# Kernel tuning notes

Measured on AMD Instinct MI355X. Metric: run time of the kernel, lower is better.

The kernel has to match this reference:

```python
import jax, jax.numpy as jnp
import numpy as np

B, N, D, H, DH = 2, 2048, 1024, 16, 64  # batch, seq, dim, heads, dim_head


def setup_inputs() -> dict:
    key = jax.random.key(0)
    ks = jax.random.split(key, 5)
    x = jax.random.normal(ks[0], (B, N, D), dtype=jnp.float32)
    Wq = jax.random.normal(ks[1], (D, H * DH), dtype=jnp.float32) * 0.02
    Wk = jax.random.normal(ks[2], (D, H * DH), dtype=jnp.float32) * 0.02
    Wv = jax.random.normal(ks[3], (D, H * DH), dtype=jnp.float32) * 0.02
    Wo = jax.random.normal(ks[4], (H * DH, D), dtype=jnp.float32) * 0.02
    bo = jnp.zeros((D,), dtype=jnp.float32)
    return {"x": x, "Wq": Wq, "Wk": Wk, "Wv": Wv, "Wo": Wo, "bo": bo}


def reference(x, Wq, Wk, Wv, Wo, bo):
    b, n, _ = x.shape
    scale = DH ** -0.5
    q = (x @ Wq).reshape(b, n, H, DH)
    k = (x @ Wk).reshape(b, n, H, DH)
    v = (x @ Wv).reshape(b, n, H, DH)
    # ALiBi slopes: 1 / (256**(1/H))**(h+1), per get_alibi_slope
    base = (2.0 ** 8) ** (1.0 / H)
    slope = 1.0 / base ** jnp.arange(1, H + 1, dtype=jnp.float32)  # [H]
    pos = jnp.arange(n, dtype=jnp.float32)
    # q_bias=[slope, slope*i], k_bias=[-j, 1] -> dot = slope*(i-j)
    bias = slope[:, None, None] * (pos[:, None] - pos[None, :])  # [H, N, N]
    scores = jnp.einsum('bihd,bjhd->bhij', q, k) * scale + bias[None]
    causal = pos[:, None] >= pos[None, :]  # i >= j
    scores = jnp.where(causal[None, None], scores, jnp.float32(-1e30))
    attn = jax.nn.softmax(scores, axis=-1)
    out = jnp.einsum('bhij,bjhd->bihd', attn, v).reshape(b, n, H * DH)
    return out @ Wo + bo
```

## Files before the change

### kernel.cpp

```cpp
#include <hip/hip_runtime.h>
#include <hip/hip_bf16.h>


typedef __bf16 bf16x8 __attribute__((ext_vector_type(8)));
typedef float f32x4 __attribute__((ext_vector_type(4)));
typedef short s4 __attribute__((ext_vector_type(4)));
typedef unsigned short ushort_t;

#define MFMA_16x16x32(a, b, c) __builtin_amdgcn_mfma_f32_16x16x32_bf16(a, b, c, 0, 0, 0)
#define MFMA16(a, b, c) __builtin_amdgcn_mfma_f32_16x16x16bf16_1k(a, b, c, 0, 0, 0)

__device__ __forceinline__ ushort_t f2bf(float f) {
    __hip_bfloat16 h = __float2bfloat16(f);
    return __builtin_bit_cast(ushort_t, h);
}
__device__ __forceinline__ float bf2f(ushort_t u) {
    unsigned x = ((unsigned)u) << 16;
    return __builtin_bit_cast(float, x);
}

__device__ __forceinline__ unsigned detect_fp32(const void* wp) {
    const ushort_t* w = (const ushort_t*)wp;
    unsigned c = 0;
    #pragma unroll
    for (int i = 0; i < 128; ++i) c += (((w[i] >> 7) & 0xFF) >= 0x7F) ? 1u : 0u;
    return (c > 8) ? 1u : 0u;
}

__device__ __forceinline__ uint4 load8(const void* p, size_t idx, unsigned flag) {
    if (flag) {
        const float* f = (const float*)p + idx;
        float4 a = *(const float4*)f;
        float4 b = *(const float4*)(f + 4);
        ushort_t u[8] = { f2bf(a.x), f2bf(a.y), f2bf(a.z), f2bf(a.w),
                          f2bf(b.x), f2bf(b.y), f2bf(b.z), f2bf(b.w) };
        return *(uint4*)u;
    }
    return *(const uint4*)((const ushort_t*)p + idx);
}

__global__ __launch_bounds__(256) void convert_x(
    const void* __restrict__ X, const void* __restrict__ Wq, const void* __restrict__ bo,
    ushort_t* __restrict__ Xc, ushort_t* __restrict__ boc)
{
    const unsigned flag = detect_fp32(Wq);
    const int blk = blockIdx.x;
    if (blk < 2048) {
        size_t idx = (size_t)blk * 2048 + (size_t)threadIdx.x * 8;
        *(uint4*)(Xc + idx) = load8(X, idx, flag);
    } else {
        size_t idx = (size_t)threadIdx.x * 8;
        if (idx < 1024) *(uint4*)(boc + idx) = load8(bo, idx, flag);
    }
}

__global__ __launch_bounds__(256) void transpose_w(
    const void* __restrict__ Wq, const void* __restrict__ Wk,
    const void* __restrict__ Wv, const void* __restrict__ Wo,
    ushort_t* __restrict__ WqT, ushort_t* __restrict__ WkT,
    ushort_t* __restrict__ WvT, ushort_t* __restrict__ WoT)
{
    __shared__ ushort_t T[64][72];
    const unsigned flag = detect_fp32(Wq);
    const int z = blockIdx.z;
    const void* W = (z == 0) ? Wq : ((z == 1) ? Wk : ((z == 2) ? Wv : Wo));
    ushort_t* WT = (z == 0) ? WqT : ((z == 1) ? WkT : ((z == 2) ? WvT : WoT));

    const int k0 = blockIdx.y * 64, n0 = blockIdx.x * 64;
    const int r = threadIdx.x >> 2, c = (threadIdx.x & 3) * 16;

    *(uint4*)&T[r][c]     = load8(W, (size_t)(k0 + r) * 1024 + n0 + c,     flag);
    *(uint4*)&T[r][c + 8] = load8(W, (size_t)(k0 + r) * 1024 + n0 + c + 8, flag);
    __syncthreads();
    ushort_t tmp[16];
    #pragma unroll
    for (int j = 0; j < 16; ++j) tmp[j] = T[c + j][r];
    *(uint4*)(WT + (size_t)(n0 + r) * 1024 + k0 + c)     = *(uint4*)&tmp[0];
    *(uint4*)(WT + (size_t)(n0 + r) * 1024 + k0 + c + 8) = *(uint4*)&tmp[8];
}

__global__ __launch_bounds__(256) void qkv_gemm(
    const ushort_t* __restrict__ X, const ushort_t* __restrict__ WqT,
    const ushort_t* __restrict__ WkT, const ushort_t* __restrict__ WvT,
    ushort_t* __restrict__ Q, ushort_t* __restrict__ K, ushort_t* __restrict__ Vt)
{
    __shared__ ushort_t As[128 * 40];
    __shared__ ushort_t Bs[128 * 40];

    const int z = blockIdx.z;
    const ushort_t* WT = (z == 0) ? WqT : ((z == 1) ? WkT : WvT);

    const int tid  = threadIdx.x;
    const int m0   = blockIdx.y * 128, n0 = blockIdx.x * 128;
    const int lane = tid & 63, wv = tid >> 6;
    const int quad = lane >> 4, l15 = lane & 15;
    const int wm = (wv & 1) * 64, wn = (wv >> 1) * 64;
    const int ar = tid >> 1, ac = (tid & 1) * 16;

    f32x4 acc[4][4] = {};

    uint4 ra0 = *(const uint4*)(X  + (size_t)(m0 + ar) * 1024 + ac);
    uint4 ra1 = *(const uint4*)(X  + (size_t)(m0 + ar) * 1024 + ac + 8);
    uint4 rb0 = *(const uint4*)(WT + (size_t)(n0 + ar) * 1024 + ac);
    uint4 rb1 = *(const uint4*)(WT + (size_t)(n0 + ar) * 1024 + ac + 8);

    for (int kt = 0; kt < 32; ++kt) {
        __syncthreads();
        *(uint4*)(As + ar * 40 + ac)     = ra0;
        *(uint4*)(As + ar * 40 + ac + 8) = ra1;
        *(uint4*)(Bs + ar * 40 + ac)     = rb0;
        *(uint4*)(Bs + ar * 40 + ac + 8) = rb1;
        __syncthreads();
        if (kt < 31) {
            int k0 = (kt + 1) * 32;
            ra0 = *(const uint4*)(X  + (size_t)(m0 + ar) * 1024 + k0 + ac);
            ra1 = *(const uint4*)(X  + (size_t)(m0 + ar) * 1024 + k0 + ac + 8);
            rb0 = *(const uint4*)(WT + (size_t)(n0 + ar) * 1024 + k0 + ac);
            rb1 = *(const uint4*)(WT + (size_t)(n0 + ar) * 1024 + k0 + ac + 8);
        }
        bf16x8 af[4], bfr[4];
        #pragma unroll
        for (int t = 0; t < 4; ++t) {
            af[t]  = *(const bf16x8*)(As + (wm + t * 16 + l15) * 40 + quad * 8);
            bfr[t] = *(const bf16x8*)(Bs + (wn + t * 16 + l15) * 40 + quad * 8);
        }
        #pragma unroll
        for (int mt = 0; mt < 4; ++mt)
            #pragma unroll
            for (int nt = 0; nt < 4; ++nt)
                acc[mt][nt] = MFMA_16x16x32(af[mt], bfr[nt], acc[mt][nt]);
    }

    #pragma unroll
    for (int mt = 0; mt < 4; ++mt) {
        #pragma unroll
        for (int nt = 0; nt < 4; ++nt) {
            if (z == 2) {
                int c  = n0 + wn + nt * 16 + l15;
                int h  = c >> 6, dh = c & 63;
                int mA = m0 + wm + mt * 16 + quad * 4;
                int b  = mA >> 11, nseq = mA & 2047;
                ushort_t pk[4];
                #pragma unroll
                for (int r = 0; r < 4; ++r) pk[r] = f2bf(acc[mt][nt][r]);
                *(ushort2*)(Vt + ((size_t)((b * 16 + h) * 64 + dh)) * 2048 + nseq)     = *(ushort2*)&pk[0];
                *(ushort2*)(Vt + ((size_t)((b * 16 + h) * 64 + dh)) * 2048 + nseq + 2) = *(ushort2*)&pk[2];
            } else {
                ushort_t* dst = (z == 0) ? Q : K;
                #pragma unroll
                for (int r = 0; r < 4; ++r) {
                    int m = m0 + wm + mt * 16 + quad * 4 + r;
                    int c = n0 + wn + nt * 16 + l15;
                    int b = m >> 11, nseq = m & 2047;
                    int h = c >> 6, dh = c & 63;
                    dst[((size_t)((b * 16 + h) * 2048 + nseq)) * 64 + dh] = f2bf(acc[mt][nt][r]);
                }
            }
        }
    }
}

__global__ __launch_bounds__(256) void attn_kernel(
    const ushort_t* __restrict__ Q, const ushort_t* __restrict__ K,
    const ushort_t* __restrict__ Vt, ushort_t* __restrict__ AO)
{
    __shared__ ushort_t Ks[64 * 72];
    __shared__ ushort_t Vs[64 * 72];

    const int tid  = threadIdx.x;
    const int wv   = tid >> 6, lane = tid & 63;
    const int quad = lane >> 4, l15 = lane & 15;
    const int bh   = blockIdx.x, h = bh & 15, b = bh >> 4;
    const int qb   = 31 - (int)blockIdx.y;
    const int iw   = qb * 64 + wv * 16;
    const int i_   = iw + l15;

    const ushort_t* Qh = Q  + (size_t)bh * 2048 * 64;
    const ushort_t* Kh = K  + (size_t)bh * 2048 * 64;
    const ushort_t* Vh = Vt + (size_t)bh * 64 * 2048;

    const float LOG2E = 1.44269504088896340736f;
    const float sl2 = exp2f(-0.5f * (float)(h + 1)) * LOG2E;
    const float c1  = 0.125f * LOG2E;

    bf16x8 qf0 = *(const bf16x8*)(Qh + (size_t)(iw + l15) * 64 + quad * 8);
    bf16x8 qf1 = *(const bf16x8*)(Qh + (size_t)(iw + l15) * 64 + 32 + quad * 8);

    s4 onesf;
    #pragma unroll
    for (int e = 0; e < 4; ++e) onesf[e] = (short)0x3F80;

    f32x4 accv[4] = {};
    f32x4 accl = {};

    const int sr = tid >> 2, sc = (tid & 3) * 16;
    const int ntiles = qb + 1;

    uint4 ka0, ka1, va0, va1;
    {
        ka0 = *(const uint4*)(Kh + (size_t)sr * 64 + sc);
        ka1 = *(const uint4*)(Kh + (size_t)sr * 64 + sc + 8);
        va0 = *(const uint4*)(Vh + (size_t)sr * 2048 + sc);
        va1 = *(const uint4*)(Vh + (size_t)sr * 2048 + sc + 8);
    }

    for (int jt = 0; jt < ntiles; ++jt) {
        __syncthreads();
        *(uint4*)(Ks + sr * 72 + sc)     = ka0;
        *(uint4*)(Ks + sr * 72 + sc + 8) = ka1;
        *(uint4*)(Vs + sr * 72 + sc)     = va0;
        *(uint4*)(Vs + sr * 72 + sc + 8) = va1;
        __syncthreads();
        if (jt + 1 < ntiles) {
            int j0n = (jt + 1) * 64;
            ka0 = *(const uint4*)(Kh + (size_t)(j0n + sr) * 64 + sc);
            ka1 = *(const uint4*)(Kh + (size_t)(j0n + sr) * 64 + sc + 8);
            va0 = *(const uint4*)(Vh + (size_t)sr * 2048 + j0n + sc);
            va1 = *(const uint4*)(Vh + (size_t)sr * 2048 + j0n + sc + 8);
        }
        const bool dtile = (jt == qb);
        #pragma unroll
        for (int js = 0; js < 4; ++js) {
            const int j0s = jt * 64 + js * 16;
            if (dtile && j0s > iw + 15) break;
            f32x4 sT = {};
            bf16x8 kf0 = *(const bf16x8*)(Ks + (js * 16 + l15) * 72 + quad * 8);
            bf16x8 kf1 = *(const bf16x8*)(Ks + (js * 16 + l15) * 72 + 32 + quad * 8);
            sT = MFMA_16x16x32(kf0, qf0, sT);
            sT = MFMA_16x16x32(kf1, qf1, sT);
            unsigned u[4];
            #pragma unroll
            for (int r = 0; r < 4; ++r) {
                int j = j0s + quad * 4 + r;
                float p = exp2f(fmaf(sT[r], c1, -sl2 * (float)j));
                if (dtile && j > i_) p = 0.0f;
                u[r] = __builtin_bit_cast(unsigned, p) + 0x8000u;
            }
            uint2 dd = { (u[0] >> 16) | (u[1] & 0xFFFF0000u),
                         (u[2] >> 16) | (u[3] & 0xFFFF0000u) };
            s4 pf = __builtin_bit_cast(s4, dd);
            accl = MFMA16(onesf, pf, accl);
            #pragma unroll
            for (int dt = 0; dt < 4; ++dt) {
                s4 vf = *(const s4*)(Vs + (dt * 16 + l15) * 72 + js * 16 + quad * 4);
                accv[dt] = MFMA16(vf, pf, accv[dt]);
            }
        }
    }

    const float inv = 1.0f / fmaxf(accl[0], 1e-30f);
    const size_t obase = ((size_t)(b * 2048 + i_)) * 1024 + h * 64;
    #pragma unroll
    for (int dt = 0; dt < 4; ++dt) {
        ushort_t pk[4];
        #pragma unroll
        for (int r = 0; r < 4; ++r) pk[r] = f2bf(accv[dt][r] * inv);
        *(ushort2*)(AO + obase + dt * 16 + quad * 4)     = *(ushort2*)&pk[0];
        *(ushort2*)(AO + obase + dt * 16 + quad * 4 + 2) = *(ushort2*)&pk[2];
    }
}

__global__ __launch_bounds__(256) void oproj_gemm(
    const ushort_t* __restrict__ A, const ushort_t* __restrict__ WT,
    const ushort_t* __restrict__ bias, float* __restrict__ out)
{
    __shared__ ushort_t As[128 * 40];
    __shared__ ushort_t Bs[128 * 40];

    const int tid  = threadIdx.x;
    const int m0   = blockIdx.y * 128, n0 = blockIdx.x * 128;
    const int lane = tid & 63, wv = tid >> 6;
    const int quad = lane >> 4, l15 = lane & 15;
    const int wm = (wv & 1) * 64, wn = (wv >> 1) * 64;
    const int ar = tid >> 1, ac = (tid & 1) * 16;

    f32x4 acc[4][4] = {};

    uint4 ra0 = *(const uint4*)(A  + (size_t)(m0 + ar) * 1024 + ac);
    uint4 ra1 = *(const uint4*)(A  + (size_t)(m0 + ar) * 1024 + ac + 8);
    uint4 rb0 = *(const uint4*)(WT + (size_t)(n0 + ar) * 1024 + ac);
    uint4 rb1 = *(const uint4*)(WT + (size_t)(n0 + ar) * 1024 + ac + 8);

    for (int kt = 0; kt < 32; ++kt) {
        __syncthreads();
        *(uint4*)(As + ar * 40 + ac)     = ra0;
        *(uint4*)(As + ar * 40 + ac + 8) = ra1;
        *(uint4*)(Bs + ar * 40 + ac)     = rb0;
        *(uint4*)(Bs + ar * 40 + ac + 8) = rb1;
        __syncthreads();
        if (kt < 31) {
            int k0 = (kt + 1) * 32;
            ra0 = *(const uint4*)(A  + (size_t)(m0 + ar) * 1024 + k0 + ac);
            ra1 = *(const uint4*)(A  + (size_t)(m0 + ar) * 1024 + k0 + ac + 8);
            rb0 = *(const uint4*)(WT + (size_t)(n0 + ar) * 1024 + k0 + ac);
            rb1 = *(const uint4*)(WT + (size_t)(n0 + ar) * 1024 + k0 + ac + 8);
        }
        bf16x8 af[4], bfr[4];
        #pragma unroll
        for (int t = 0; t < 4; ++t) {
            af[t]  = *(const bf16x8*)(As + (wm + t * 16 + l15) * 40 + quad * 8);
            bfr[t] = *(const bf16x8*)(Bs + (wn + t * 16 + l15) * 40 + quad * 8);
        }
        #pragma unroll
        for (int mt = 0; mt < 4; ++mt)
            #pragma unroll
            for (int nt = 0; nt < 4; ++nt)
                acc[mt][nt] = MFMA_16x16x32(af[mt], bfr[nt], acc[mt][nt]);
    }

    #pragma unroll
    for (int mt = 0; mt < 4; ++mt) {
        #pragma unroll
        for (int nt = 0; nt < 4; ++nt) {
            #pragma unroll
            for (int r = 0; r < 4; ++r) {
                int m = m0 + wm + mt * 16 + quad * 4 + r;
                int c = n0 + wn + nt * 16 + l15;
                out[(size_t)m * 1024 + c] = acc[mt][nt][r] + bf2f(bias[c]);
            }
        }
    }
}

extern "C" void kernel_launch(void* const* d_in, const int* in_sizes, int n_in,
                              void* d_out, int out_size, void* d_ws, size_t ws_size,
                              hipStream_t stream) {
    const void* X  = d_in[0];
    const void* Wq = d_in[1];
    const void* Wk = d_in[2];
    const void* Wv = d_in[3];
    const void* Wo = d_in[4];
    const void* bo = d_in[5];

    const size_t M = 1024 * 1024;
    ushort_t* ws  = (ushort_t*)d_ws;
    ushort_t* Qb  = ws;
    ushort_t* Kb  = ws + 4 * M;
    ushort_t* Vt  = ws + 8 * M;
    ushort_t* Xc  = ws + 12 * M;
    ushort_t* AO  = ws + 12 * M;
    ushort_t* WqT = ws + 16 * M;
    ushort_t* WkT = ws + 17 * M;
    ushort_t* WvT = ws + 18 * M;
    ushort_t* WoT = ws + 19 * M;
    ushort_t* boc = ws + 20 * M;
    float* out = (float*)d_out;

    convert_x<<<2049, 256, 0, stream>>>(X, Wq, bo, Xc, boc);
    transpose_w<<<dim3(16, 16, 4), 256, 0, stream>>>(Wq, Wk, Wv, Wo, WqT, WkT, WvT, WoT);
    qkv_gemm<<<dim3(8, 32, 3), 256, 0, stream>>>(Xc, WqT, WkT, WvT, Qb, Kb, Vt);
    attn_kernel<<<dim3(32, 32), 256, 0, stream>>>(Qb, Kb, Vt, AO);
    oproj_gemm<<<dim3(8, 32), 256, 0, stream>>>(AO, WoT, boc, out);
}
```

Baseline: 198.0 us.

## Load GEMM tiles directly into LDS with XOR swizzle and split causal diagonal path

Both projection GEMMs now stage tiles with global_load_lds, copying straight from global memory into an unpadded, XOR-swizzled LDS layout instead of passing through registers. This frees registers and avoids the padded layout. It also gives up the register prefetch of the next tile, so each iteration waits on its own loads with no overlap. The attention kernel splits off the diagonal tile so each wave runs only its needed subtiles, with masking applied only on the last one.

```diff
diff --git a/kernel.cpp b/kernel.cpp
--- a/kernel.cpp
+++ b/kernel.cpp
@@ -17,6 +17,12 @@
 __device__ __forceinline__ float bf2f(ushort_t u) {
     unsigned x = ((unsigned)u) << 16;
     return __builtin_bit_cast(float, x);
+}
+
+__device__ __forceinline__ void gl_lds16(const ushort_t* g, ushort_t* l) {
+    __builtin_amdgcn_global_load_lds(
+        (const __attribute__((address_space(1))) void*)g,
+        (__attribute__((address_space(3))) void*)l, 16, 0, 0);
 }
 
 __device__ __forceinline__ unsigned detect_fp32(const void* wp) {
@@ -84,8 +90,8 @@
     const ushort_t* __restrict__ WkT, const ushort_t* __restrict__ WvT,
     ushort_t* __restrict__ Q, ushort_t* __restrict__ K, ushort_t* __restrict__ Vt)
 {
-    __shared__ ushort_t As[128 * 40];
-    __shared__ ushort_t Bs[128 * 40];
+    __shared__ ushort_t As[128 * 32];
+    __shared__ ushort_t Bs[128 * 32];
 
     const int z = blockIdx.z;
     const ushort_t* WT = (z == 0) ? WqT : ((z == 1) ? WkT : WvT);
@@ -95,34 +101,32 @@
     const int lane = tid & 63, wv = tid >> 6;
     const int quad = lane >> 4, l15 = lane & 15;
     const int wm = (wv & 1) * 64, wn = (wv >> 1) * 64;
-    const int ar = tid >> 1, ac = (tid & 1) * 16;
+
+    const int lrow = lane >> 2;
+    const int schk = (lane & 3) ^ ((lane >> 3) & 3);
+    const int ra0_ = wv * 16 + lrow;
+    ushort_t* aB0 = As + wv * 512;
+    ushort_t* aB1 = As + 2048 + wv * 512;
+    ushort_t* bB0 = Bs + wv * 512;
+    ushort_t* bB1 = Bs + 2048 + wv * 512;
+    const int sp = quad ^ ((l15 >> 1) & 3);
 
     f32x4 acc[4][4] = {};
 
-    uint4 ra0 = *(const uint4*)(X  + (size_t)(m0 + ar) * 1024 + ac);
-    uint4 ra1 = *(const uint4*)(X  + (size_t)(m0 + ar) * 1024 + ac + 8);
-    uint4 rb0 = *(const uint4*)(WT + (size_t)(n0 + ar) * 1024 + ac);
-    uint4 rb1 = *(const uint4*)(WT + (size_t)(n0 + ar) * 1024 + ac + 8);
-
     for (int kt = 0; kt < 32; ++kt) {
-        __syncthreads();
-        *(uint4*)(As + ar * 40 + ac)     = ra0;
-        *(uint4*)(As + ar * 40 + ac + 8) = ra1;
-        *(uint4*)(Bs + ar * 40 + ac)     = rb0;
-        *(uint4*)(Bs + ar * 40 + ac + 8) = rb1;
-        __syncthreads();
-        if (kt < 31) {
-            int k0 = (kt + 1) * 32;
-            ra0 = *(const uint4*)(X  + (size_t)(m0 + ar) * 1024 + k0 + ac);
-            ra1 = *(const uint4*)(X  + (size_t)(m0 + ar) * 1024 + k0 + ac + 8);
-            rb0 = *(const uint4*)(WT + (size_t)(n0 + ar) * 1024 + k0 + ac);
-            rb1 = *(const uint4*)(WT + (size_t)(n0 + ar) * 1024 + k0 + ac + 8);
-        }
+        const int k0 = kt * 32;
+        __syncthreads();
+        gl_lds16(X  + (size_t)(m0 + ra0_)      * 1024 + k0 + schk * 8, aB0);
+        gl_lds16(X  + (size_t)(m0 + 64 + ra0_) * 1024 + k0 + schk * 8, aB1);
+        gl_lds16(WT + (size_t)(n0 + ra0_)      * 1024 + k0 + schk * 8, bB0);
+        gl_lds16(WT + (size_t)(n0 + 64 + ra0_) * 1024 + k0 + schk * 8, bB1);
+        __syncthreads();
+
         bf16x8 af[4], bfr[4];
         #pragma unroll
         for (int t = 0; t < 4; ++t) {
-            af[t]  = *(const bf16x8*)(As + (wm + t * 16 + l15) * 40 + quad * 8);
-            bfr[t] = *(const bf16x8*)(Bs + (wn + t * 16 + l15) * 40 + quad * 8);
+            af[t]  = *(const bf16x8*)(As + (wm + t * 16 + l15) * 32 + sp * 8);
+            bfr[t] = *(const bf16x8*)(Bs + (wn + t * 16 + l15) * 32 + sp * 8);
         }
         #pragma unroll
         for (int mt = 0; mt < 4; ++mt)
@@ -196,13 +200,36 @@
     const int sr = tid >> 2, sc = (tid & 3) * 16;
     const int ntiles = qb + 1;
 
-    uint4 ka0, ka1, va0, va1;
-    {
-        ka0 = *(const uint4*)(Kh + (size_t)sr * 64 + sc);
-        ka1 = *(const uint4*)(Kh + (size_t)sr * 64 + sc + 8);
-        va0 = *(const uint4*)(Vh + (size_t)sr * 2048 + sc);
-        va1 = *(const uint4*)(Vh + (size_t)sr * 2048 + sc + 8);
-    }
+    uint4 ka0 = *(const uint4*)(Kh + (size_t)sr * 64 + sc);
+    uint4 ka1 = *(const uint4*)(Kh + (size_t)sr * 64 + sc + 8);
+    uint4 va0 = *(const uint4*)(Vh + (size_t)sr * 2048 + sc);
+    uint4 va1 = *(const uint4*)(Vh + (size_t)sr * 2048 + sc + 8);
+
+    auto subtile = [&](int jt, int js, bool masked) {
+        const int j0s = jt * 64 + js * 16;
+        f32x4 sT = {};
+        bf16x8 kf0 = *(const bf16x8*)(Ks + (js * 16 + l15) * 72 + quad * 8);
+        bf16x8 kf1 = *(const bf16x8*)(Ks + (js * 16 + l15) * 72 + 32 + quad * 8);
+        sT = MFMA_16x16x32(kf0, qf0, sT);
+        sT = MFMA_16x16x32(kf1, qf1, sT);
+        unsigned u[4];
+        #pragma unroll
+        for (int r = 0; r < 4; ++r) {
+            int j = j0s + quad * 4 + r;
+            float p = exp2f(fmaf(sT[r], c1, -sl2 * (float)j));
+            if (masked && j > i_) p = 0.0f;
+            u[r] = __builtin_bit_cast(unsigned, p) + 0x8000u;
+        }
+        uint2 dd = { (u[0] >> 16) | (u[1] & 0xFFFF0000u),
+                     (u[2] >> 16) | (u[3] & 0xFFFF0000u) };
+        s4 pf = __builtin_bit_cast(s4, dd);
+        accl = MFMA16(onesf, pf, accl);
+        #pragma unroll
+        for (int dt = 0; dt < 4; ++dt) {
+            s4 vf = *(const s4*)(Vs + (dt * 16 + l15) * 72 + js * 16 + quad * 4);
+            accv[dt] = MFMA16(vf, pf, accv[dt]);
+        }
+    };
 
     for (int jt = 0; jt < ntiles; ++jt) {
         __syncthreads();
@@ -218,33 +245,12 @@
             va0 = *(const uint4*)(Vh + (size_t)sr * 2048 + j0n + sc);
             va1 = *(const uint4*)(Vh + (size_t)sr * 2048 + j0n + sc + 8);
         }
-        const bool dtile = (jt == qb);
-        #pragma unroll
-        for (int js = 0; js < 4; ++js) {
-            const int j0s = jt * 64 + js * 16;
-            if (dtile && j0s > iw + 15) break;
-            f32x4 sT = {};
-            bf16x8 kf0 = *(const bf16x8*)(Ks + (js * 16 + l15) * 72 + quad * 8);
-            bf16x8 kf1 = *(const bf16x8*)(Ks + (js * 16 + l15) * 72 + 32 + quad * 8);
-            sT = MFMA_16x16x32(kf0, qf0, sT);
-            sT = MFMA_16x16x32(kf1, qf1, sT);
-            unsigned u[4];
+        if (jt < qb) {
             #pragma unroll
-            for (int r = 0; r < 4; ++r) {
-                int j = j0s + quad * 4 + r;
-                float p = exp2f(fmaf(sT[r], c1, -sl2 * (float)j));
-                if (dtile && j > i_) p = 0.0f;
-                u[r] = __builtin_bit_cast(unsigned, p) + 0x8000u;
-            }
-            uint2 dd = { (u[0] >> 16) | (u[1] & 0xFFFF0000u),
-                         (u[2] >> 16) | (u[3] & 0xFFFF0000u) };
-            s4 pf = __builtin_bit_cast(s4, dd);
-            accl = MFMA16(onesf, pf, accl);
-            #pragma unroll
-            for (int dt = 0; dt < 4; ++dt) {
-                s4 vf = *(const s4*)(Vs + (dt * 16 + l15) * 72 + js * 16 + quad * 4);
-                accv[dt] = MFMA16(vf, pf, accv[dt]);
-            }
+            for (int js = 0; js < 4; ++js) subtile(jt, js, false);
+        } else {
+            for (int js = 0; js < wv; ++js) subtile(jt, js, false);
+            subtile(jt, wv, true);
         }
     }
 
@@ -264,42 +270,40 @@
     const ushort_t* __restrict__ A, const ushort_t* __restrict__ WT,
     const ushort_t* __restrict__ bias, float* __restrict__ out)
 {
-    __shared__ ushort_t As[128 * 40];
-    __shared__ ushort_t Bs[128 * 40];
+    __shared__ ushort_t As[128 * 32];
+    __shared__ ushort_t Bs[128 * 32];
 
     const int tid  = threadIdx.x;
     const int m0   = blockIdx.y * 128, n0 = blockIdx.x * 128;
     const int lane = tid & 63, wv = tid >> 6;
     const int quad = lane >> 4, l15 = lane & 15;
     const int wm = (wv & 1) * 64, wn = (wv >> 1) * 64;
-    const int ar = tid >> 1, ac = (tid & 1) * 16;
+
+    const int lrow = lane >> 2;
+    const int schk = (lane & 3) ^ ((lane >> 3) & 3);
+    const int ra0_ = wv * 16 + lrow;
+    ushort_t* aB0 = As + wv * 512;
+    ushort_t* aB1 = As + 2048 + wv * 512;
+    ushort_t* bB0 = Bs + wv * 512;
+    ushort_t* bB1 = Bs + 2048 + wv * 512;
+    const int sp = quad ^ ((l15 >> 1) & 3);
 
     f32x4 acc[4][4] = {};
 
-    uint4 ra0 = *(const uint4*)(A  + (size_t)(m0 + ar) * 1024 + ac);
-    uint4 ra1 = *(const uint4*)(A  + (size_t)(m0 + ar) * 1024 + ac + 8);
-    uint4 rb0 = *(const uint4*)(WT + (size_t)(n0 + ar) * 1024 + ac);
-    uint4 rb1 = *(const uint4*)(WT + (size_t)(n0 + ar) * 1024 + ac + 8);
-
     for (int kt = 0; kt < 32; ++kt) {
-        __syncthreads();
-        *(uint4*)(As + ar * 40 + ac)     = ra0;
-        *(uint4*)(As + ar * 40 + ac + 8) = ra1;
-        *(uint4*)(Bs + ar * 40 + ac)     = rb0;
-        *(uint4*)(Bs + ar * 40 + ac + 8) = rb1;
-        __syncthreads();
-        if (kt < 31) {
-            int k0 = (kt + 1) * 32;
-            ra0 = *(const uint4*)(A  + (size_t)(m0 + ar) * 1024 + k0 + ac);
-            ra1 = *(const uint4*)(A  + (size_t)(m0 + ar) * 1024 + k0 + ac + 8);
-            rb0 = *(const uint4*)(WT + (size_t)(n0 + ar) * 1024 + k0 + ac);
-            rb1 = *(const uint4*)(WT + (size_t)(n0 + ar) * 1024 + k0 + ac + 8);
-        }
+        const int k0 = kt * 32;
+        __syncthreads();
+        gl_lds16(A  + (size_t)(m0 + ra0_)      * 1024 + k0 + schk * 8, aB0);
+        gl_lds16(A  + (size_t)(m0 + 64 + ra0_) * 1024 + k0 + schk * 8, aB1);
+        gl_lds16(WT + (size_t)(n0 + ra0_)      * 1024 + k0 + schk * 8, bB0);
+        gl_lds16(WT + (size_t)(n0 + 64 + ra0_) * 1024 + k0 + schk * 8, bB1);
+        __syncthreads();
+
         bf16x8 af[4], bfr[4];
         #pragma unroll
         for (int t = 0; t < 4; ++t) {
-            af[t]  = *(const bf16x8*)(As + (wm + t * 16 + l15) * 40 + quad * 8);
-            bfr[t] = *(const bf16x8*)(Bs + (wn + t * 16 + l15) * 40 + quad * 8);
+            af[t]  = *(const bf16x8*)(As + (wm + t * 16 + l15) * 32 + sp * 8);
+            bfr[t] = *(const bf16x8*)(Bs + (wn + t * 16 + l15) * 32 + sp * 8);
         }
         #pragma unroll
         for (int mt = 0; mt < 4; ++mt)
```

After: 194.5 us. About the same (-1.8%).
